# Optimization experiments

Hardware: AMD Instinct MI355X
Metric: run time of the kernel (lower is better)

The kernel has to match this reference:

```python
import jax, jax.numpy as jnp
import numpy as np

B, T, D, H, L = 256, 256, 64, 512, 2


def setup_inputs() -> dict:
    key = jax.random.key(0)
    ks = jax.random.split(key, 12)
    s = 1.0 / np.sqrt(H)
    u = lambda k, shp: jax.random.uniform(k, shp, jnp.float32, -s, s)
    return {
        "x": jax.random.normal(ks[0], (B, T, D), jnp.float32),
        "W_ih0": u(ks[1], (4 * H, D)),
        "W_hh0": u(ks[2], (4 * H, H)),
        "b_ih0": u(ks[3], (4 * H,)),
        "b_hh0": u(ks[4], (4 * H,)),
        "W_ih1": u(ks[5], (4 * H, H)),
        "W_hh1": u(ks[6], (4 * H, H)),
        "b_ih1": u(ks[7], (4 * H,)),
        "b_hh1": u(ks[8], (4 * H,)),
        "fc_w": u(ks[9], (1, H)),
        "fc_b": u(ks[10], (1,)),
    }


def _lstm_layer(xs, W_ih, W_hh, b):
    # xs: [T, B, Din] -> hs: [T, B, H]. PyTorch gate order: i, f, g, o.
    Wt, Ut = W_ih.T, W_hh.T
    # precompute input contribution for all timesteps (one big GEMM)
    gx = jnp.einsum("tbd,df->tbf", xs, Wt) + b  # [T, B, 4H]

    def step(carry, gxt):
        h, c = carry
        g = gxt + h @ Ut
        i, f, gg, o = jnp.split(g, 4, axis=-1)
        c = jax.nn.sigmoid(f) * c + jax.nn.sigmoid(i) * jnp.tanh(gg)
        h = jax.nn.sigmoid(o) * jnp.tanh(c)
        return (h, c), h

    Bn = xs.shape[1]
    init = (jnp.zeros((Bn, W_hh.shape[1]), xs.dtype), jnp.zeros((Bn, W_hh.shape[1]), xs.dtype))
    _, hs = jax.lax.scan(step, init, gx)
    return hs


def reference(x, W_ih0, W_hh0, b_ih0, b_hh0, W_ih1, W_hh1, b_ih1, b_hh1, fc_w, fc_b):
    xs = jnp.transpose(x, (1, 0, 2))  # [T, B, D]
    h1 = _lstm_layer(xs, W_ih0, W_hh0, b_ih0 + b_hh0)
    h2 = _lstm_layer(h1, W_ih1, W_hh1, b_ih1 + b_hh1)
    last = h2[-1]  # [B, H] == out[:, -1]
    return last @ fc_w.T + fc_b  # [B, 1]
```

## Files before the change

### kernel.cpp

```cpp
#include <hip/hip_runtime.h>

#define Bb 256
#define Tt 256
#define Dd 64
#define Hh 512
#define BH (Bb*Hh)
#define S1 6

typedef _Float16 half8 __attribute__((ext_vector_type(8)));
typedef float floatx4 __attribute__((ext_vector_type(4)));
typedef unsigned long long u64x2 __attribute__((ext_vector_type(2)));

__device__ __forceinline__ float sigm(float x) { return 1.0f/(1.0f + __expf(-x)); }
__device__ __forceinline__ float tanh_(float x) {
  if (x >  15.0f) return  1.0f;
  if (x < -15.0f) return -1.0f;
  float e = __expf(2.0f*x);
  return (e - 1.0f)/(e + 1.0f);
}

__device__ __forceinline__ void st_u64(_Float16* p, unsigned long long v) {
  __hip_atomic_store((unsigned long long*)p, v, __ATOMIC_RELAXED, __HIP_MEMORY_SCOPE_AGENT);
}
__device__ __forceinline__ half8 ld_h8(const _Float16* p) {
  u64x2 t;
  t.x = __hip_atomic_load((const unsigned long long*)p,       __ATOMIC_RELAXED, __HIP_MEMORY_SCOPE_AGENT);
  t.y = __hip_atomic_load(((const unsigned long long*)p) + 1, __ATOMIC_RELAXED, __HIP_MEMORY_SCOPE_AGENT);
  return __builtin_bit_cast(half8, t);
}
__device__ __forceinline__ unsigned ld_flag(const unsigned* p) {
  return __hip_atomic_load(p, __ATOMIC_RELAXED, __HIP_MEMORY_SCOPE_AGENT);
}
__device__ __forceinline__ void st_flag(unsigned* p, unsigned v) {
  __hip_atomic_store(p, v, __ATOMIC_RELAXED, __HIP_MEMORY_SCOPE_AGENT);
}

#define LD16(A) \
    "global_load_dwordx4 %0, " A ", off sc0 sc1\n\t" \
    "global_load_dwordx4 %1, " A ", off offset:64 sc0 sc1\n\t" \
    "global_load_dwordx4 %2, " A ", off offset:128 sc0 sc1\n\t" \
    "global_load_dwordx4 %3, " A ", off offset:192 sc0 sc1\n\t" \
    "global_load_dwordx4 %4, " A ", off offset:256 sc0 sc1\n\t" \
    "global_load_dwordx4 %5, " A ", off offset:320 sc0 sc1\n\t" \
    "global_load_dwordx4 %6, " A ", off offset:384 sc0 sc1\n\t" \
    "global_load_dwordx4 %7, " A ", off offset:448 sc0 sc1\n\t" \
    "global_load_dwordx4 %8, " A ", off offset:512 sc0 sc1\n\t" \
    "global_load_dwordx4 %9, " A ", off offset:576 sc0 sc1\n\t" \
    "global_load_dwordx4 %10, " A ", off offset:640 sc0 sc1\n\t" \
    "global_load_dwordx4 %11, " A ", off offset:704 sc0 sc1\n\t" \
    "global_load_dwordx4 %12, " A ", off offset:768 sc0 sc1\n\t" \
    "global_load_dwordx4 %13, " A ", off offset:832 sc0 sc1\n\t" \
    "global_load_dwordx4 %14, " A ", off offset:896 sc0 sc1\n\t" \
    "global_load_dwordx4 %15, " A ", off offset:960 sc0 sc1\n\t"
#define LD16OUT(o) \
      "=&v"(o[0]),"=&v"(o[1]),"=&v"(o[2]),"=&v"(o[3]), \
      "=&v"(o[4]),"=&v"(o[5]),"=&v"(o[6]),"=&v"(o[7]), \
      "=&v"(o[8]),"=&v"(o[9]),"=&v"(o[10]),"=&v"(o[11]), \
      "=&v"(o[12]),"=&v"(o[13]),"=&v"(o[14]),"=&v"(o[15])

__device__ __forceinline__ void ld16_batch(const _Float16* p, half8 o[16]) {
  asm volatile(LD16("%16") "s_waitcnt vmcnt(0)"
    : LD16OUT(o) : "v"(p) : "memory");
}

__global__ void init_kernel(unsigned long long* __restrict__ hz,
                            unsigned* __restrict__ flags) {
  const int j0 = blockIdx.x*blockDim.x + threadIdx.x;
  if (j0 < 512) flags[j0] = 0u;
  const int NZ = (S1 + 3)*BH/4;
  for (int j = j0; j < NZ; j += gridDim.x*blockDim.x) hz[j] = 0ull;
}

__global__ void __launch_bounds__(256, 1)
lstm_fused(const float* __restrict__ x,
           _Float16* __restrict__ hb,
           unsigned* __restrict__ flags,
           const float* __restrict__ Wih0, const float* __restrict__ Whh0,
           const float* __restrict__ bih0, const float* __restrict__ bhh0,
           const float* __restrict__ Wih1, const float* __restrict__ Whh1,
           const float* __restrict__ bih1, const float* __restrict__ bhh1,
           const float* __restrict__ fcw,  const float* __restrict__ fcb,
           float* __restrict__ out)
{
  extern __shared__ _Float16 lds[];

  const int tid = threadIdx.x;
  const int bid = blockIdx.x;
  const int grp = bid & 7;
  const int lb  = grp >> 2;
  const int rgi = grp & 3;
  const int cgi = bid >> 3;
  const int hc0 = cgi * 16;
  const int r0  = rgi * 64;

  unsigned* const myexp = flags + grp*32 + cgi;

  _Float16* const h1e = hb;
  _Float16* const h2l = hb + S1*BH;
  _Float16* const h2e = hb + (S1 + 2)*BH;

  {
    const float* Whh = lb ? Whh1 : Whh0;
    const float* Wih = lb ? Wih1 : Wih0;
    const int Kin = lb ? Hh : Dd;
    const int KT  = Hh + Kin;
    for (int idx = tid; idx < 64*KT; idx += 256) {
      const int gr = idx / KT;
      const int k  = idx - gr*KT;
      const int bt = gr >> 4, s = gr & 15;
      const int gate = (bt & 1)*2 + (s >> 3);
      const int hcc  = (bt >> 1)*8 + (s & 7);
      const int wrow = gate*Hh + hc0 + hcc;
      const float v = (k < Hh) ? Whh[(size_t)wrow*Hh + k]
                               : Wih[(size_t)wrow*Kin + (k - Hh)];
      const int li = (((k >> 5)*4 + bt) << 9) + ((((k >> 3) & 3)*16 + s) << 3) + (k & 7);
      lds[li] = (_Float16)v;
    }
  }
  __syncthreads();

  const int w    = tid >> 6;
  const int lane = tid & 63;
  const int kg   = lane >> 4;
  const int n15  = lane & 15;
  const bool lo  = (n15 < 8);
  const int rowb = r0 + w*16;

  const _Float16* const bfrag = lds + (lane << 3);
  _Float16* const stage = lds + 65536 + w*256;
  const size_t stoff = (size_t)(rowb + (lane >> 2))*Hh + hc0 + (lane & 3)*4;
  const size_t rowoff = (size_t)(rowb + n15)*Hh + 8*kg;

  const float* bi = lb ? bih1 : bih0;
  const float* bh = lb ? bhh1 : bhh0;
  float biasA[2], biasB[2];
  #pragma unroll
  for (int o = 0; o < 2; ++o) {
    const int hc = hc0 + o*8 + (n15 & 7);
    biasA[o] = lo ? (bi[hc]      + bh[hc])      : (bi[512+hc]  + bh[512+hc]);
    biasB[o] = lo ? (bi[1024+hc] + bh[1024+hc]) : (bi[1536+hc] + bh[1536+hc]);
  }

  float cst[2][4] = {{0.f,0.f,0.f,0.f},{0.f,0.f,0.f,0.f}};

  for (int i = 0; i <= Tt; ++i) {
    const bool active = lb ? (i >= 1) : (i < Tt);
    if (active) {
      floatx4 acc[4] = {};

      if (lb) {
        if (tid < 32) {
          const unsigned* fp = flags + (grp ^ 4)*32 + tid;
          while (!__all((int)(ld_flag(fp) >= (unsigned)i)))
            __builtin_amdgcn_s_sleep(1);
        }
        __syncthreads();
        __builtin_amdgcn_sched_barrier(0);
        {
          const _Float16* cp = h1e + (size_t)((i+S1-1)%S1)*BH + rowoff;
          half8 a2[16];
          ld16_batch(cp, a2);
          #pragma unroll
          for (int ks = 0; ks < 16; ++ks)
            #pragma unroll
            for (int bt = 0; bt < 4; ++bt)
              acc[bt] = __builtin_amdgcn_mfma_f32_16x16x32_f16(
                          a2[ks], *(const half8*)(bfrag + (((16+ks)*4 + bt) << 9)), acc[bt], 0,0,0);
        }
        if (tid < 32) {
          const unsigned* fp = flags + grp*32 + tid;
          while (!__all((int)(ld_flag(fp) >= (unsigned)i)))
            __builtin_amdgcn_s_sleep(1);
        }
        __syncthreads();
        __builtin_amdgcn_sched_barrier(0);
        {
          const _Float16* ap = h2l + (size_t)((i+1)&1)*BH + rowoff;
          half8 a1[16];
          ld16_batch(ap, a1);
          #pragma unroll
          for (int ks = 0; ks < 16; ++ks)
            #pragma unroll
            for (int bt = 0; bt < 4; ++bt)
              acc[bt] = __builtin_amdgcn_mfma_f32_16x16x32_f16(
                          a1[ks], *(const half8*)(bfrag + ((ks*4 + bt) << 9)), acc[bt], 0,0,0);
        }
      } else {
        const float* xp = x + (((size_t)(rowb + n15)) << 14) + ((size_t)i << 6) + 8*kg;
        const floatx4 xa = *(const floatx4*)(xp);
        const floatx4 xb = *(const floatx4*)(xp + 4);
        const floatx4 xc = *(const floatx4*)(xp + 32);
        const floatx4 xd = *(const floatx4*)(xp + 36);
        if (tid < 64) {
          const int m = tid & 31;
          const bool self = (tid < 32);
          const unsigned tgt = self ? (unsigned)i
                                    : ((i >= S1) ? (unsigned)(i - (S1 - 2)) : 0u);
          const unsigned* fp = flags + (self ? grp : (grp ^ 4))*32 + m;
          while (!__all((int)(ld_flag(fp) >= tgt)))
            __builtin_amdgcn_s_sleep(1);
        }
        __syncthreads();
        __builtin_amdgcn_sched_barrier(0);
        const _Float16* ap = h1e + (size_t)((i+S1-1)%S1)*BH + rowoff;
        half8 a1[16];
        ld16_batch(ap, a1);
        half8 a2[2];
        #pragma unroll
        for (int e = 0; e < 4; ++e) {
          a2[0][e] = (_Float16)xa[e]; a2[0][4+e] = (_Float16)xb[e];
          a2[1][e] = (_Float16)xc[e]; a2[1][4+e] = (_Float16)xd[e];
        }
        #pragma unroll
        for (int ks = 0; ks < 16; ++ks)
          #pragma unroll
          for (int bt = 0; bt < 4; ++bt)
            acc[bt] = __builtin_amdgcn_mfma_f32_16x16x32_f16(
                        a1[ks], *(const half8*)(bfrag + ((ks*4 + bt) << 9)), acc[bt], 0,0,0);
        #pragma unroll
        for (int ks = 0; ks < 2; ++ks)
          #pragma unroll
          for (int bt = 0; bt < 4; ++bt)
            acc[bt] = __builtin_amdgcn_mfma_f32_16x16x32_f16(
                        a2[ks], *(const half8*)(bfrag + (((16+ks)*4 + bt) << 9)), acc[bt], 0,0,0);
      }

      #pragma unroll
      for (int o = 0; o < 2; ++o) {
        #pragma unroll
        for (int rr = 0; rr < 4; ++rr) {
          const float pA = acc[2*o][rr]   + biasA[o];
          const float pB = acc[2*o+1][rr] + biasB[o];
          const float v1 = sigm(pA);
          const float v2 = lo ? tanh_(pB) : sigm(pB);
          const float fs  = __shfl_xor(v1, 8, 64);
          const float os_ = __shfl_xor(v2, 8, 64);
          if (lo) {
            const float c = fs * cst[o][rr] + v1 * v2;
            cst[o][rr] = c;
            stage[(kg*4 + rr)*16 + o*8 + (n15 & 7)] = (_Float16)(os_ * tanh_(c));
          }
        }
      }
      asm volatile("s_waitcnt lgkmcnt(0)" ::: "memory");
      __builtin_amdgcn_sched_barrier(0);
      const unsigned long long pk = *(const unsigned long long*)(stage + (lane << 2));

      if (!lb) {
        st_u64(h1e + (size_t)(i%S1)*BH + stoff, pk);
      } else {
        st_u64(h2l + (size_t)(i&1)*BH + stoff, pk);
        if (i == Tt) st_u64(h2e + stoff, pk);
      }
    }

    asm volatile("s_waitcnt vmcnt(0)" ::: "memory");
    __syncthreads();
    if (tid == 0) st_flag(myexp, (unsigned)(i + 1));
  }

  if (bid == 0) {
    if (tid < 64) {
      const unsigned* f1 = flags + (4 + (tid >> 5))*32 + (tid & 31);
      const unsigned* f2 = f1 + 64;
      while (1) {
        int ok = (ld_flag(f1) > (unsigned)Tt) & (ld_flag(f2) > (unsigned)Tt);
        if (__all(ok)) break;
        __builtin_amdgcn_s_sleep(1);
      }
    }
    __syncthreads();
    asm volatile("" ::: "memory");
    float acc = fcb[0];
    for (int c = 0; c < 4; ++c) {
      half8 v[16];
      #pragma unroll
      for (int j = 0; j < 16; ++j)
        v[j] = ld_h8(h2e + (size_t)tid*Hh + c*128 + j*8);
      #pragma unroll
      for (int j = 0; j < 16; ++j)
        #pragma unroll
        for (int e = 0; e < 8; ++e)
          acc += (float)v[j][e] * fcw[c*128 + j*8 + e];
    }
    out[tid] = acc;
  }
}

extern "C" void kernel_launch(void* const* d_in, const int* in_sizes, int n_in,
                              void* d_out, int out_size, void* d_ws, size_t ws_size,
                              hipStream_t stream) {
  const float* x    = (const float*)d_in[0];
  const float* Wih0 = (const float*)d_in[1];
  const float* Whh0 = (const float*)d_in[2];
  const float* bih0 = (const float*)d_in[3];
  const float* bhh0 = (const float*)d_in[4];
  const float* Wih1 = (const float*)d_in[5];
  const float* Whh1 = (const float*)d_in[6];
  const float* bih1 = (const float*)d_in[7];
  const float* bhh1 = (const float*)d_in[8];
  const float* fcw  = (const float*)d_in[9];
  const float* fcb  = (const float*)d_in[10];
  float* out = (float*)d_out;

  _Float16* hb    = (_Float16*)d_ws;
  unsigned* flags = (unsigned*)(hb + (size_t)(S1 + 3)*BH);

  hipFuncSetAttribute((const void*)lstm_fused,
                      hipFuncAttributeMaxDynamicSharedMemorySize, 133120);

  hipLaunchKernelGGL(init_kernel, dim3(512), dim3(256), 0, stream,
                     (unsigned long long*)hb, flags);

  hipLaunchKernelGGL(lstm_fused, dim3(256), dim3(256), 133120, stream,
                     x, hb, flags,
                     Wih0, Whh0, bih0, bhh0, Wih1, Whh1, bih1, bhh1, fcw, fcb, out);
}
```

Baseline: 2.394 ms.

## Halve persistent grid with 32 hidden columns per block, stream W_ih from global

```diff
diff --git a/kernel.cpp b/kernel.cpp
--- a/kernel.cpp
+++ b/kernel.cpp
@@ -63,21 +63,47 @@
     : LD16OUT(o) : "v"(p) : "memory");
 }
 
-__global__ void init_kernel(unsigned long long* __restrict__ hz,
+__global__ void init_kernel(const float* __restrict__ Wih0,
+                            const float* __restrict__ Wih1,
+                            unsigned long long* __restrict__ hz,
+                            _Float16* __restrict__ wf0,
+                            _Float16* __restrict__ wf1,
                             unsigned* __restrict__ flags) {
   const int j0 = blockIdx.x*blockDim.x + threadIdx.x;
+  const int stride = gridDim.x*blockDim.x;
   if (j0 < 512) flags[j0] = 0u;
   const int NZ = (S1 + 3)*BH/4;
-  for (int j = j0; j < NZ; j += gridDim.x*blockDim.x) hz[j] = 0ull;
+  for (int j = j0; j < NZ; j += stride) hz[j] = 0ull;
+  for (int j = j0; j < 131072; j += stride) {
+    const int e = j & 7, l = (j >> 3) & 63, bt = (j >> 9) & 7;
+    const int ks = (j >> 12) & 1, cgi = j >> 13;
+    const int kg = l >> 4, s = l & 15;
+    const int k = 32*ks + 8*kg + e;
+    const int gate = (bt & 1)*2 + (s >> 3);
+    const int hcc  = (bt >> 1)*8 + (s & 7);
+    const int wrow = gate*Hh + cgi*32 + hcc;
+    wf0[j] = (_Float16)Wih0[(size_t)wrow*Dd + k];
+  }
+  for (int j = j0; j < 1048576; j += stride) {
+    const int e = j & 7, l = (j >> 3) & 63, bt = (j >> 9) & 7;
+    const int ks = (j >> 12) & 15, cgi = j >> 16;
+    const int kg = l >> 4, s = l & 15;
+    const int k = 32*ks + 8*kg + e;
+    const int gate = (bt & 1)*2 + (s >> 3);
+    const int hcc  = (bt >> 1)*8 + (s & 7);
+    const int wrow = gate*Hh + cgi*32 + hcc;
+    wf1[j] = (_Float16)Wih1[(size_t)wrow*Hh + k];
+  }
 }
 
 __global__ void __launch_bounds__(256, 1)
 lstm_fused(const float* __restrict__ x,
            _Float16* __restrict__ hb,
+           const _Float16* __restrict__ wf0,
+           const _Float16* __restrict__ wf1,
            unsigned* __restrict__ flags,
-           const float* __restrict__ Wih0, const float* __restrict__ Whh0,
+           const float* __restrict__ Whh0, const float* __restrict__ Whh1,
            const float* __restrict__ bih0, const float* __restrict__ bhh0,
-           const float* __restrict__ Wih1, const float* __restrict__ Whh1,
            const float* __restrict__ bih1, const float* __restrict__ bhh1,
            const float* __restrict__ fcw,  const float* __restrict__ fcb,
            float* __restrict__ out)
@@ -90,7 +116,7 @@
   const int lb  = grp >> 2;
   const int rgi = grp & 3;
   const int cgi = bid >> 3;
-  const int hc0 = cgi * 16;
+  const int hc0 = cgi * 32;
   const int r0  = rgi * 64;
 
   unsigned* const myexp = flags + grp*32 + cgi;
@@ -101,20 +127,14 @@
 
   {
     const float* Whh = lb ? Whh1 : Whh0;
-    const float* Wih = lb ? Wih1 : Wih0;
-    const int Kin = lb ? Hh : Dd;
-    const int KT  = Hh + Kin;
-    for (int idx = tid; idx < 64*KT; idx += 256) {
-      const int gr = idx / KT;
-      const int k  = idx - gr*KT;
+    for (int idx = tid; idx < 128*512; idx += 256) {
+      const int gr = idx >> 9, k = idx & 511;
       const int bt = gr >> 4, s = gr & 15;
       const int gate = (bt & 1)*2 + (s >> 3);
       const int hcc  = (bt >> 1)*8 + (s & 7);
       const int wrow = gate*Hh + hc0 + hcc;
-      const float v = (k < Hh) ? Whh[(size_t)wrow*Hh + k]
-                               : Wih[(size_t)wrow*Kin + (k - Hh)];
-      const int li = (((k >> 5)*4 + bt) << 9) + ((((k >> 3) & 3)*16 + s) << 3) + (k & 7);
-      lds[li] = (_Float16)v;
+      const int li = (((k >> 5)*8 + bt) << 9) + ((((k >> 3) & 3)*16 + s) << 3) + (k & 7);
+      lds[li] = (_Float16)Whh[(size_t)wrow*Hh + k];
     }
   }
   __syncthreads();
@@ -127,30 +147,32 @@
   const int rowb = r0 + w*16;
 
   const _Float16* const bfrag = lds + (lane << 3);
-  _Float16* const stage = lds + 65536 + w*256;
-  const size_t stoff = (size_t)(rowb + (lane >> 2))*Hh + hc0 + (lane & 3)*4;
+  _Float16* const stage = lds + 65536 + w*512;
   const size_t rowoff = (size_t)(rowb + n15)*Hh + 8*kg;
+  const size_t stoff  = (size_t)(rowb + (lane >> 2))*Hh + hc0 + (lane & 3)*4;
+  const _Float16* const wfrag = (lb ? (wf1 + ((size_t)cgi << 16))
+                                    : (wf0 + ((size_t)cgi << 13))) + (lane << 3);
 
   const float* bi = lb ? bih1 : bih0;
   const float* bh = lb ? bhh1 : bhh0;
-  float biasA[2], biasB[2];
+  float biasA[4], biasB[4];
   #pragma unroll
-  for (int o = 0; o < 2; ++o) {
+  for (int o = 0; o < 4; ++o) {
     const int hc = hc0 + o*8 + (n15 & 7);
     biasA[o] = lo ? (bi[hc]      + bh[hc])      : (bi[512+hc]  + bh[512+hc]);
     biasB[o] = lo ? (bi[1024+hc] + bh[1024+hc]) : (bi[1536+hc] + bh[1536+hc]);
   }
 
-  float cst[2][4] = {{0.f,0.f,0.f,0.f},{0.f,0.f,0.f,0.f}};
+  float cst[4][4] = {};
 
   for (int i = 0; i <= Tt; ++i) {
     const bool active = lb ? (i >= 1) : (i < Tt);
     if (active) {
-      floatx4 acc[4] = {};
+      floatx4 acc[8] = {};
 
       if (lb) {
         if (tid < 32) {
-          const unsigned* fp = flags + (grp ^ 4)*32 + tid;
+          const unsigned* fp = flags + (grp ^ 4)*32 + (tid & 15);
           while (!__all((int)(ld_flag(fp) >= (unsigned)i)))
             __builtin_amdgcn_s_sleep(1);
         }
@@ -163,12 +185,13 @@
           #pragma unroll
           for (int ks = 0; ks < 16; ++ks)
             #pragma unroll
-            for (int bt = 0; bt < 4; ++bt)
-              acc[bt] = __builtin_amdgcn_mfma_f32_16x16x32_f16(
-                          a2[ks], *(const half8*)(bfrag + (((16+ks)*4 + bt) << 9)), acc[bt], 0,0,0);
+            for (int bt = 0; bt < 8; ++bt) {
+              const half8 wv = *(const half8*)(wfrag + ((ks*8 + bt) << 9));
+              acc[bt] = __builtin_amdgcn_mfma_f32_16x16x32_f16(a2[ks], wv, acc[bt], 0,0,0);
+            }
         }
         if (tid < 32) {
-          const unsigned* fp = flags + grp*32 + tid;
+          const unsigned* fp = flags + grp*32 + (tid & 15);
           while (!__all((int)(ld_flag(fp) >= (unsigned)i)))
             __builtin_amdgcn_s_sleep(1);
         }
@@ -181,9 +204,9 @@
           #pragma unroll
           for (int ks = 0; ks < 16; ++ks)
             #pragma unroll
-            for (int bt = 0; bt < 4; ++bt)
+            for (int bt = 0; bt < 8; ++bt)
               acc[bt] = __builtin_amdgcn_mfma_f32_16x16x32_f16(
-                          a1[ks], *(const half8*)(bfrag + ((ks*4 + bt) << 9)), acc[bt], 0,0,0);
+                          a1[ks], *(const half8*)(bfrag + ((ks*8 + bt) << 9)), acc[bt], 0,0,0);
         }
       } else {
         const float* xp = x + (((size_t)(rowb + n15)) << 14) + ((size_t)i << 6) + 8*kg;
@@ -196,7 +219,7 @@
           const bool self = (tid < 32);
           const unsigned tgt = self ? (unsigned)i
                                     : ((i >= S1) ? (unsigned)(i - (S1 - 2)) : 0u);
-          const unsigned* fp = flags + (self ? grp : (grp ^ 4))*32 + m;
+          const unsigned* fp = flags + (self ? grp : (grp ^ 4))*32 + (m & 15);
           while (!__all((int)(ld_flag(fp) >= tgt)))
             __builtin_amdgcn_s_sleep(1);
         }
@@ -214,19 +237,20 @@
         #pragma unroll
         for (int ks = 0; ks < 16; ++ks)
           #pragma unroll
-          for (int bt = 0; bt < 4; ++bt)
+          for (int bt = 0; bt < 8; ++bt)
             acc[bt] = __builtin_amdgcn_mfma_f32_16x16x32_f16(
-                        a1[ks], *(const half8*)(bfrag + ((ks*4 + bt) << 9)), acc[bt], 0,0,0);
+                        a1[ks], *(const half8*)(bfrag + ((ks*8 + bt) << 9)), acc[bt], 0,0,0);
         #pragma unroll
         for (int ks = 0; ks < 2; ++ks)
           #pragma unroll
-          for (int bt = 0; bt < 4; ++bt)
-            acc[bt] = __builtin_amdgcn_mfma_f32_16x16x32_f16(
-                        a2[ks], *(const half8*)(bfrag + (((16+ks)*4 + bt) << 9)), acc[bt], 0,0,0);
+          for (int bt = 0; bt < 8; ++bt) {
+            const half8 wv = *(const half8*)(wfrag + ((ks*8 + bt) << 9));
+            acc[bt] = __builtin_amdgcn_mfma_f32_16x16x32_f16(a2[ks], wv, acc[bt], 0,0,0);
+          }
       }
 
       #pragma unroll
-      for (int o = 0; o < 2; ++o) {
+      for (int o = 0; o < 4; ++o) {
         #pragma unroll
         for (int rr = 0; rr < 4; ++rr) {
           const float pA = acc[2*o][rr]   + biasA[o];
@@ -238,19 +262,24 @@
           if (lo) {
             const float c = fs * cst[o][rr] + v1 * v2;
             cst[o][rr] = c;
-            stage[(kg*4 + rr)*16 + o*8 + (n15 & 7)] = (_Float16)(os_ * tanh_(c));
+            stage[(kg*4 + rr)*32 + o*8 + (n15 & 7)] = (_Float16)(os_ * tanh_(c));
           }
         }
       }
       asm volatile("s_waitcnt lgkmcnt(0)" ::: "memory");
       __builtin_amdgcn_sched_barrier(0);
-      const unsigned long long pk = *(const unsigned long long*)(stage + (lane << 2));
+      const unsigned long long pk0 = *(const unsigned long long*)(stage + (lane >> 2)*32 + (lane & 3)*4);
+      const unsigned long long pk1 = *(const unsigned long long*)(stage + (lane >> 2)*32 + 16 + (lane & 3)*4);
 
       if (!lb) {
-        st_u64(h1e + (size_t)(i%S1)*BH + stoff, pk);
+        _Float16* hc = h1e + (size_t)(i%S1)*BH;
+        st_u64(hc + stoff, pk0);
+        st_u64(hc + stoff + 16, pk1);
       } else {
-        st_u64(h2l + (size_t)(i&1)*BH + stoff, pk);
-        if (i == Tt) st_u64(h2e + stoff, pk);
+        _Float16* hc = h2l + (size_t)(i&1)*BH;
+        st_u64(hc + stoff, pk0);
+        st_u64(hc + stoff + 16, pk1);
+        if (i == Tt) { st_u64(h2e + stoff, pk0); st_u64(h2e + stoff + 16, pk1); }
       }
     }
 
@@ -261,13 +290,9 @@
 
   if (bid == 0) {
     if (tid < 64) {
-      const unsigned* f1 = flags + (4 + (tid >> 5))*32 + (tid & 31);
-      const unsigned* f2 = f1 + 64;
-      while (1) {
-        int ok = (ld_flag(f1) > (unsigned)Tt) & (ld_flag(f2) > (unsigned)Tt);
-        if (__all(ok)) break;
+      const unsigned* fp = flags + (4 + (tid >> 4))*32 + (tid & 15);
+      while (!__all((int)(ld_flag(fp) > (unsigned)Tt)))
         __builtin_amdgcn_s_sleep(1);
-      }
     }
     __syncthreads();
     asm volatile("" ::: "memory");
@@ -304,15 +329,17 @@
   float* out = (float*)d_out;
 
   _Float16* hb    = (_Float16*)d_ws;
-  unsigned* flags = (unsigned*)(hb + (size_t)(S1 + 3)*BH);
+  _Float16* wf0   = hb + (size_t)(S1 + 3)*BH;
+  _Float16* wf1   = wf0 + 131072;
+  unsigned* flags = (unsigned*)(wf1 + 1048576);
 
   hipFuncSetAttribute((const void*)lstm_fused,
-                      hipFuncAttributeMaxDynamicSharedMemorySize, 133120);
+                      hipFuncAttributeMaxDynamicSharedMemorySize, 135168);
 
   hipLaunchKernelGGL(init_kernel, dim3(512), dim3(256), 0, stream,
-                     (unsigned long long*)hb, flags);
-
-  hipLaunchKernelGGL(lstm_fused, dim3(256), dim3(256), 133120, stream,
-                     x, hb, flags,
-                     Wih0, Whh0, bih0, bhh0, Wih1, Whh1, bih1, bhh1, fcw, fcb, out);
-}
+                     Wih0, Wih1, (unsigned long long*)hb, wf0, wf1, flags);
+
+  hipLaunchKernelGGL(lstm_fused, dim3(128), dim3(256), 135168, stream,
+                     x, hb, (const _Float16*)wf0, (const _Float16*)wf1, flags,
+                     Whh0, Whh1, bih0, bhh0, bih1, bhh1, fcw, fcb, out);
+}
```

After: 6.459 ms. 2.7x slower.
